# Optimization experiments

Measured on AMD Instinct MI355X. Metric: run time of the kernel, lower is better.

The kernel has to match this reference:

```python
import jax, jax.numpy as jnp
import numpy as np

N_NODES = 100000
N_EDGES = 3200000
D_NODE = 128
D_EDGE = 16


def setup_inputs() -> dict:
    key = jax.random.key(0)
    k1, k2, k3, k4, k5, k6, k7 = jax.random.split(key, 7)
    nodes = jax.random.normal(k1, (N_NODES, D_NODE), dtype=jnp.float32)
    edges = jax.random.normal(k2, (N_EDGES, D_EDGE), dtype=jnp.float32)
    senders = jax.random.randint(k3, (N_EDGES,), 0, N_NODES, dtype=jnp.int32)
    receivers = jax.random.randint(k4, (N_EDGES,), 0, N_NODES, dtype=jnp.int32)
    w_node = jax.random.normal(k5, (), dtype=jnp.float32)
    w_edge = jax.random.normal(k6, (), dtype=jnp.float32)
    b_node = jax.random.normal(k7, (), dtype=jnp.float32)
    return {
        "nodes": nodes,
        "edges": edges,
        "senders": senders,
        "receivers": receivers,
        "w_node": w_node,
        "w_edge": w_edge,
        "b_node": b_node,
    }


def reference(nodes, edges, senders, receivers, w_node, w_edge, b_node):
    # gather sender node scalar feature (column 0): [E]
    sender_vals = nodes[senders, 0]
    edge_vals = edges[:, 0]  # [E]
    # per-edge message: scalar mult-add
    messages = w_edge * edge_vals + w_node * sender_vals  # [E]
    # scatter-add into receivers: [N]
    agg = jax.ops.segment_sum(messages, receivers, num_segments=nodes.shape[0])
    return w_node * nodes[:, 0] + agg + b_node
```

## Files before the change

kernel.cpp:

```cpp
#include <hip/hip_runtime.h>

#define N_NODES 100000
#define N_EDGES 3200000
#define D_NODE 128
#define D_EDGE 16

#define NR 7
#define SPAN 16384
#define CAP 560000
#define NSLICE 64

#define K1_THREADS 512
#define K1_EDGES 1024

#define WS_X     0
#define WS_CNT   100000
#define WS_OVF   100008
#define WS_BKT   200008
#define WS_PART  (WS_BKT + NR * CAP * 2)
#define WS_TOTAL (WS_PART + NSLICE * N_NODES)

typedef int   iv2 __attribute__((ext_vector_type(2)));
typedef int   iv4 __attribute__((ext_vector_type(4)));
typedef float fv4 __attribute__((ext_vector_type(4)));

__global__ void v3_init(const float* __restrict__ nodes,
                        float* __restrict__ x,
                        float* __restrict__ ovf,
                        int*   __restrict__ cnt) {
    int i = blockIdx.x * blockDim.x + threadIdx.x;
    if (i < 8) cnt[i] = 0;
    if (i < N_NODES) {
        x[i]   = nodes[(size_t)i * D_NODE];
        ovf[i] = 0.f;
    }
}

__global__ __launch_bounds__(K1_THREADS) void v3_bucketize(
        const float* __restrict__ x,
        const float* __restrict__ edges,
        const int*   __restrict__ senders,
        const int*   __restrict__ receivers,
        const float* __restrict__ w_node,
        const float* __restrict__ w_edge,
        int*   __restrict__ cnt,
        float* __restrict__ ovf,
        int*   __restrict__ bkt) {
    __shared__ int   s_loc[NR * K1_EDGES];
    __shared__ float s_msg[NR * K1_EDGES];
    __shared__ int   s_lcnt[NR], s_gbase[NR], s_offs[NR + 1];

    const float wn = w_node[0];
    const float we = w_edge[0];
    const int tile = blockIdx.x * K1_EDGES;

    if (threadIdx.x < NR) s_lcnt[threadIdx.x] = 0;
    __syncthreads();

    int rr[2]; float mm[2];
#pragma unroll
    for (int j = 0; j < 2; ++j) {
        int e = tile + j * K1_THREADS + (int)threadIdx.x;
        rr[j]    = __builtin_nontemporal_load(receivers + e);
        int s    = __builtin_nontemporal_load(senders + e);
        float ev = __builtin_nontemporal_load(edges + (size_t)e * D_EDGE);
        mm[j] = we * ev + wn * x[s];
    }
#pragma unroll
    for (int j = 0; j < 2; ++j) {
        int b   = rr[j] >> 14;
        int pos = atomicAdd(&s_lcnt[b], 1);
        s_loc[b * K1_EDGES + pos] = rr[j] & (SPAN - 1);
        s_msg[b * K1_EDGES + pos] = mm[j];
    }
    __syncthreads();

    if (threadIdx.x < NR)
        s_gbase[threadIdx.x] = atomicAdd(&cnt[threadIdx.x], s_lcnt[threadIdx.x]);
    if (threadIdx.x == 0) {
        int o = 0;
        for (int b = 0; b < NR; ++b) { s_offs[b] = o; o += s_lcnt[b]; }
        s_offs[NR] = o;
    }
    __syncthreads();

    const int tot = s_offs[NR];
    for (int i = threadIdx.x; i < tot; i += K1_THREADS) {
        int b = 0;
        while (i >= s_offs[b + 1]) ++b;
        int k   = i - s_offs[b];
        int gi  = s_gbase[b] + k;
        int loc = s_loc[b * K1_EDGES + k];
        float m = s_msg[b * K1_EDGES + k];
        if (gi < CAP) {
            iv2 v; v.x = loc; v.y = __float_as_int(m);
            *(iv2*)(bkt + ((size_t)b * CAP + gi) * 2) = v;
        } else {
            atomicAdd(&ovf[b * SPAN + loc], m);
        }
    }
}

__global__ __launch_bounds__(1024) void v3_accum(
        const int* __restrict__ bkt,
        const int* __restrict__ cnt,
        float* __restrict__ partials) {
    extern __shared__ float acc[];
    const int r  = blockIdx.y;
    const int lo = r * SPAN;
    int span = N_NODES - lo; if (span > SPAN) span = SPAN;

    const int n     = cnt[r];
    const int chunk = (n + NSLICE - 1) / NSLICE;
    int start = blockIdx.x * chunk;
    int end   = start + chunk; if (end > n) end = n;

    for (int i = threadIdx.x * 4; i < SPAN; i += 4096) {
        fv4 z = {0.f, 0.f, 0.f, 0.f};
        *(fv4*)(acc + i) = z;
    }
    __syncthreads();

    const int* base = bkt + (size_t)r * CAP * 2;
    for (int i = start + (int)threadIdx.x; i < end; i += 1024) {
        iv2 v = *(const iv2*)(base + (size_t)i * 2);
        atomicAdd(&acc[v.x], __int_as_float(v.y));
    }
    __syncthreads();

    float* dst = partials + (size_t)blockIdx.x * N_NODES + lo;
    for (int i = threadIdx.x * 4; i < span; i += 4096)
        *(fv4*)(dst + i) = *(const fv4*)(acc + i);
}

__global__ void v3_out(const float* __restrict__ x,
                       const float* __restrict__ partials,
                       const float* __restrict__ ovf,
                       const float* __restrict__ w_node,
                       const float* __restrict__ b_node,
                       float* __restrict__ out) {
    int i = blockIdx.x * blockDim.x + threadIdx.x;
    if (i >= N_NODES) return;
    float s = w_node[0] * x[i] + b_node[0] + ovf[i];
#pragma unroll 8
    for (int c = 0; c < NSLICE; ++c) s += partials[(size_t)c * N_NODES + i];
    out[i] = s;
}

__global__ void tmp_init_out(const float* __restrict__ nodes,
                             const float* __restrict__ w_node,
                             const float* __restrict__ b_node,
                             float* __restrict__ out) {
    int i = blockIdx.x * blockDim.x + threadIdx.x;
    if (i < N_NODES) out[i] = w_node[0] * nodes[(size_t)i * D_NODE] + b_node[0];
}

__global__ void tmp_edge_scatter_direct(const float* __restrict__ nodes,
                                        const float* __restrict__ edges,
                                        const int*   __restrict__ senders,
                                        const int*   __restrict__ receivers,
                                        const float* __restrict__ w_node,
                                        const float* __restrict__ w_edge,
                                        float* __restrict__ out) {
    const float wn = w_node[0];
    const float we = w_edge[0];
    int base = (blockIdx.x * blockDim.x + threadIdx.x) * 4;
    if (base + 3 < N_EDGES) {
        iv4 s = *(const iv4*)(senders + base);
        iv4 r = *(const iv4*)(receivers + base);
        atomicAdd(&out[r.x], we * edges[(size_t)(base + 0) * D_EDGE] + wn * nodes[(size_t)s.x * D_NODE]);
        atomicAdd(&out[r.y], we * edges[(size_t)(base + 1) * D_EDGE] + wn * nodes[(size_t)s.y * D_NODE]);
        atomicAdd(&out[r.z], we * edges[(size_t)(base + 2) * D_EDGE] + wn * nodes[(size_t)s.z * D_NODE]);
        atomicAdd(&out[r.w], we * edges[(size_t)(base + 3) * D_EDGE] + wn * nodes[(size_t)s.w * D_NODE]);
    } else {
        for (int e = base; e < N_EDGES; ++e) {
            atomicAdd(&out[receivers[e]],
                      we * edges[(size_t)e * D_EDGE] + wn * nodes[(size_t)senders[e] * D_NODE]);
        }
    }
}

extern "C" void kernel_launch(void* const* d_in, const int* in_sizes, int n_in,
                              void* d_out, int out_size, void* d_ws, size_t ws_size,
                              hipStream_t stream) {
    const float* nodes     = (const float*)d_in[0];
    const float* edges     = (const float*)d_in[1];
    const int*   senders   = (const int*)d_in[2];
    const int*   receivers = (const int*)d_in[3];
    const float* w_node    = (const float*)d_in[4];
    const float* w_edge    = (const float*)d_in[5];
    const float* b_node    = (const float*)d_in[6];
    float* out = (float*)d_out;
    float* ws  = (float*)d_ws;

    if (ws_size >= (size_t)WS_TOTAL * sizeof(float)) {
        float* x    = ws + WS_X;
        int*   cnt  = (int*)(ws + WS_CNT);
        float* ovf  = ws + WS_OVF;
        int*   bkt  = (int*)(ws + WS_BKT);
        float* part = ws + WS_PART;

        int threads = 256;
        v3_init<<<(N_NODES + threads - 1) / threads, threads, 0, stream>>>(
            nodes, x, ovf, cnt);

        v3_bucketize<<<N_EDGES / K1_EDGES, K1_THREADS, 0, stream>>>(
            x, edges, senders, receivers, w_node, w_edge, cnt, ovf, bkt);

        dim3 grid2(NSLICE, NR);
        v3_accum<<<grid2, 1024, SPAN * sizeof(float), stream>>>(bkt, cnt, part);

        v3_out<<<(N_NODES + threads - 1) / threads, threads, 0, stream>>>(
            x, part, ovf, w_node, b_node, out);
    } else {
        int threads = 256;
        tmp_init_out<<<(N_NODES + threads - 1) / threads, threads, 0, stream>>>(
            nodes, w_node, b_node, out);
        int n_thr = N_EDGES / 4;
        tmp_edge_scatter_direct<<<(n_thr + threads - 1) / threads, threads, 0, stream>>>(
            nodes, edges, senders, receivers, w_node, w_edge, out);
    }
}
```

Baseline: 367.2 us.

## Replace shared-atomic bucketing with wave-ballot ranking and per-bucket coalesced writes

The bucketize kernel now ranks each edge within its bucket using wave ballots and popcounts plus per-wave prefix offsets, instead of shared-memory atomics. Bucket entries are packed as int2 pairs in shared memory, and each bucket is written out in a contiguous loop, which removes the per-element bucket search. The block size also drops to 256 threads and 512 edges, giving more, smaller blocks. The cost is several block-wide barriers per round and a loop of seven ballots.

```diff
diff --git a/kernel.cpp b/kernel.cpp
--- a/kernel.cpp
+++ b/kernel.cpp
@@ -10,8 +10,10 @@
 #define CAP 560000
 #define NSLICE 64
 
-#define K1_THREADS 512
-#define K1_EDGES 1024
+#define K1_THREADS 256
+#define K1_EDGES 512
+#define NW (K1_THREADS / 64)
+#define K1_ROUNDS (K1_EDGES / K1_THREADS)
 
 #define WS_X     0
 #define WS_CNT   100000
@@ -24,7 +26,7 @@
 typedef int   iv4 __attribute__((ext_vector_type(4)));
 typedef float fv4 __attribute__((ext_vector_type(4)));
 
-__global__ void v3_init(const float* __restrict__ nodes,
+__global__ void v4_init(const float* __restrict__ nodes,
                         float* __restrict__ x,
                         float* __restrict__ ovf,
                         int*   __restrict__ cnt) {
@@ -36,7 +38,7 @@
     }
 }
 
-__global__ __launch_bounds__(K1_THREADS) void v3_bucketize(
+__global__ __launch_bounds__(K1_THREADS) void v4_bucketize(
         const float* __restrict__ x,
         const float* __restrict__ edges,
         const int*   __restrict__ senders,
@@ -46,62 +48,80 @@
         int*   __restrict__ cnt,
         float* __restrict__ ovf,
         int*   __restrict__ bkt) {
-    __shared__ int   s_loc[NR * K1_EDGES];
-    __shared__ float s_msg[NR * K1_EDGES];
-    __shared__ int   s_lcnt[NR], s_gbase[NR], s_offs[NR + 1];
+    __shared__ iv2 s_pair[NR][K1_EDGES];
+    __shared__ int s_wcnt[NW][NR];
+    __shared__ int s_wbase[NW][NR];
+    __shared__ int s_fill[NR];
+    __shared__ int s_gbase[NR];
 
     const float wn = w_node[0];
     const float we = w_edge[0];
     const int tile = blockIdx.x * K1_EDGES;
-
-    if (threadIdx.x < NR) s_lcnt[threadIdx.x] = 0;
-    __syncthreads();
-
-    int rr[2]; float mm[2];
-#pragma unroll
-    for (int j = 0; j < 2; ++j) {
-        int e = tile + j * K1_THREADS + (int)threadIdx.x;
+    const int lane = threadIdx.x & 63;
+    const int wv   = threadIdx.x >> 6;
+    const unsigned long long lt = (1ull << lane) - 1ull;
+
+    if (threadIdx.x < NR) s_fill[threadIdx.x] = 0;
+
+    int rr[K1_ROUNDS]; float mm[K1_ROUNDS];
+#pragma unroll
+    for (int j = 0; j < K1_ROUNDS; ++j) {
+        int e    = tile + j * K1_THREADS + (int)threadIdx.x;
         rr[j]    = __builtin_nontemporal_load(receivers + e);
         int s    = __builtin_nontemporal_load(senders + e);
         float ev = __builtin_nontemporal_load(edges + (size_t)e * D_EDGE);
         mm[j] = we * ev + wn * x[s];
     }
-#pragma unroll
-    for (int j = 0; j < 2; ++j) {
-        int b   = rr[j] >> 14;
-        int pos = atomicAdd(&s_lcnt[b], 1);
-        s_loc[b * K1_EDGES + pos] = rr[j] & (SPAN - 1);
-        s_msg[b * K1_EDGES + pos] = mm[j];
-    }
-    __syncthreads();
+    __syncthreads();
+
+#pragma unroll
+    for (int j = 0; j < K1_ROUNDS; ++j) {
+        const int b = rr[j] >> 14;
+        int rank = 0, wcount = 0;
+#pragma unroll
+        for (int k = 0; k < NR; ++k) {
+            unsigned long long mk = __ballot(b == k);
+            if (k == b)    rank   = __popcll(mk & lt);
+            if (lane == k) wcount = __popcll(mk);
+        }
+        if (lane < NR) s_wcnt[wv][lane] = wcount;
+        __syncthreads();
+        if (threadIdx.x < NR) {
+            int bb = threadIdx.x;
+            int base = s_fill[bb];
+#pragma unroll
+            for (int w = 0; w < NW; ++w) { s_wbase[w][bb] = base; base += s_wcnt[w][bb]; }
+            s_fill[bb] = base;
+        }
+        __syncthreads();
+        iv2 v; v.x = rr[j] & (SPAN - 1); v.y = __float_as_int(mm[j]);
+        s_pair[b][s_wbase[wv][b] + rank] = v;
+        __syncthreads();
+    }
 
     if (threadIdx.x < NR)
-        s_gbase[threadIdx.x] = atomicAdd(&cnt[threadIdx.x], s_lcnt[threadIdx.x]);
-    if (threadIdx.x == 0) {
-        int o = 0;
-        for (int b = 0; b < NR; ++b) { s_offs[b] = o; o += s_lcnt[b]; }
-        s_offs[NR] = o;
-    }
-    __syncthreads();
-
-    const int tot = s_offs[NR];
-    for (int i = threadIdx.x; i < tot; i += K1_THREADS) {
-        int b = 0;
-        while (i >= s_offs[b + 1]) ++b;
-        int k   = i - s_offs[b];
-        int gi  = s_gbase[b] + k;
-        int loc = s_loc[b * K1_EDGES + k];
-        float m = s_msg[b * K1_EDGES + k];
-        if (gi < CAP) {
-            iv2 v; v.x = loc; v.y = __float_as_int(m);
-            *(iv2*)(bkt + ((size_t)b * CAP + gi) * 2) = v;
+        s_gbase[threadIdx.x] = atomicAdd(&cnt[threadIdx.x], s_fill[threadIdx.x]);
+    __syncthreads();
+
+#pragma unroll
+    for (int b = 0; b < NR; ++b) {
+        const int n  = s_fill[b];
+        const int gb = s_gbase[b];
+        if (gb + n <= CAP) {
+            for (int i = threadIdx.x; i < n; i += K1_THREADS)
+                *(iv2*)(bkt + ((size_t)b * CAP + gb + i) * 2) = s_pair[b][i];
         } else {
-            atomicAdd(&ovf[b * SPAN + loc], m);
-        }
-    }
-}
-
-__global__ __launch_bounds__(1024) void v3_accum(
+            for (int i = threadIdx.x; i < n; i += K1_THREADS) {
+                iv2 v = s_pair[b][i];
+                int gi = gb + i;
+                if (gi < CAP) *(iv2*)(bkt + ((size_t)b * CAP + gi) * 2) = v;
+                else atomicAdd(&ovf[b * SPAN + v.x], __int_as_float(v.y));
+            }
+        }
+    }
+}
+
+__global__ __launch_bounds__(1024) void v4_accum(
         const int* __restrict__ bkt,
         const int* __restrict__ cnt,
         float* __restrict__ partials) {
@@ -133,7 +153,7 @@
         *(fv4*)(dst + i) = *(const fv4*)(acc + i);
 }
 
-__global__ void v3_out(const float* __restrict__ x,
+__global__ void v4_out(const float* __restrict__ x,
                        const float* __restrict__ partials,
                        const float* __restrict__ ovf,
                        const float* __restrict__ w_node,
@@ -201,16 +221,16 @@
         float* part = ws + WS_PART;
 
         int threads = 256;
-        v3_init<<<(N_NODES + threads - 1) / threads, threads, 0, stream>>>(
+        v4_init<<<(N_NODES + threads - 1) / threads, threads, 0, stream>>>(
             nodes, x, ovf, cnt);
 
-        v3_bucketize<<<N_EDGES / K1_EDGES, K1_THREADS, 0, stream>>>(
+        v4_bucketize<<<N_EDGES / K1_EDGES, K1_THREADS, 0, stream>>>(
             x, edges, senders, receivers, w_node, w_edge, cnt, ovf, bkt);
 
         dim3 grid2(NSLICE, NR);
-        v3_accum<<<grid2, 1024, SPAN * sizeof(float), stream>>>(bkt, cnt, part);
-
-        v3_out<<<(N_NODES + threads - 1) / threads, threads, 0, stream>>>(
+        v4_accum<<<grid2, 1024, SPAN * sizeof(float), stream>>>(bkt, cnt, part);
+
+        v4_out<<<(N_NODES + threads - 1) / threads, threads, 0, stream>>>(
             x, part, ovf, w_node, b_node, out);
     } else {
         int threads = 256;
```

Result: slower. 389.6 us (+6.1%).
